# Performance work log

Hardware: AMD Instinct MI355X
Metric: run time of the kernel (lower is better)

Reference implementation:

```python
import jax, jax.numpy as jnp
import numpy as np
import math

NUM_LAYERS = 2
D_MODEL = 512
NUM_HEADS = 8
DFF = 2048
TIME_DIM = 8
B = 8
L = 512


def _ffn2(t, w1, b1, w2, b2):
    # gsm_ffn: two Dense(time_dim) layers, both with relu
    h = jax.nn.relu(t @ w1 + b1)
    return jax.nn.relu(h @ w2 + b2)


def _layer_norm(x, g, b, eps=1e-6):
    m = jnp.mean(x, axis=-1, keepdims=True)
    v = jnp.mean(jnp.square(x - m), axis=-1, keepdims=True)
    return (x - m) / jnp.sqrt(v + eps) * g + b


def _forward(x, t, wq, bq, wk, bk, wv, bv, wo, bo, w1, b1, w2, b2,
             ln1g, ln1b, ln2g, ln2b, pw1, pb1, pw2, pb2,
             sw1, sb1, sw2, sb2, bw1, bb1, bw2, bb2):
    Bn, Ln, D = x.shape
    H = NUM_HEADS
    dh = D // H
    scale = jnp.sqrt(jnp.float32(dh))
    two_pi = jnp.float32(2.0 * math.pi)
    for i in range(NUM_LAYERS):
        # ---- TimeGSMKernel: Gibbs spectral-mixture time kernel [B,L,L] ----
        pv = _ffn2(t, pw1[i], pb1[i], pw2[i], pb2[i])            # [B,L,td]
        tp = two_pi * pv * t                                      # [B,L,td]
        cos_enc = jnp.cos(tp[:, :, None, :] - tp[:, None, :, :])  # [B,L,L,td]
        sg = _ffn2(t, sw1[i], sb1[i], sw2[i], sb2[i]) + 1e-6      # [B,L,td]
        sq = sg[:, :, None, :]                                    # [B,L,1,td]
        sk = sg[:, None, :, :]                                    # [B,1,L,td]
        denom = sq * sq + sk * sk
        diff = t[:, :, None, :] - t[:, None, :, :]                # [B,L,L,1]
        exp_enc = jnp.exp(-(diff * diff) / denom)                 # [B,L,L,td]
        local_enc = jnp.sqrt(2.0 * sq * sk / denom)
        be = _ffn2(t, bw1[i], bb1[i], bw2[i], bb2[i])             # [B,L,td]
        kern = jnp.sum(be[:, :, None, :] * be[:, None, :, :]
                       * local_enc * exp_enc * cos_enc, axis=-1)  # [B,L,L]

        # ---- multi-head self-attention with kernel bias ----
        def heads(z):
            return z.reshape(Bn, Ln, H, dh).transpose(0, 2, 1, 3)
        q = heads(x @ wq[i] + bq[i])
        k = heads(x @ wk[i] + bk[i])
        v = heads(x @ wv[i] + bv[i])
        logits = jnp.einsum('bhqd,bhkd->bhqk', q, k) / scale
        logits = logits + (kern / jnp.exp(scale))[:, None, :, :]
        aw = jax.nn.softmax(logits, axis=-1)
        ctx = jnp.einsum('bhqk,bhkd->bhqd', aw, v)
        ctx = ctx.transpose(0, 2, 1, 3).reshape(Bn, Ln, D)
        attn_out = ctx @ wo[i] + bo[i]
        x = _layer_norm(x + attn_out, ln1g[i], ln1b[i])
        # ---- pointwise FFN (relu then linear) ----
        f = jax.nn.relu(x @ w1[i] + b1[i]) @ w2[i] + b2[i]
        x = _layer_norm(x + f, ln2g[i], ln2b[i])
    return x


def setup_inputs() -> dict:
    key = jax.random.key(0)
    ks = iter(jax.random.split(key, 40))
    def nrm(shape, s=0.02):
        return (jax.random.normal(next(ks), shape) * s).astype(jnp.float32)
    NL, D, TD = NUM_LAYERS, D_MODEL, TIME_DIM
    d = {
        'x': jax.random.normal(next(ks), (B, L, D), dtype=jnp.float32),
        't': jax.random.uniform(next(ks), (B, L, 1), dtype=jnp.float32),
        'wq': nrm((NL, D, D)), 'bq': jnp.zeros((NL, D), jnp.float32),
        'wk': nrm((NL, D, D)), 'bk': jnp.zeros((NL, D), jnp.float32),
        'wv': nrm((NL, D, D)), 'bv': jnp.zeros((NL, D), jnp.float32),
        'wo': nrm((NL, D, D)), 'bo': jnp.zeros((NL, D), jnp.float32),
        'w1': nrm((NL, D, DFF)), 'b1': jnp.zeros((NL, DFF), jnp.float32),
        'w2': nrm((NL, DFF, D)), 'b2': jnp.zeros((NL, D), jnp.float32),
        'ln1g': jnp.ones((NL, D), jnp.float32), 'ln1b': jnp.zeros((NL, D), jnp.float32),
        'ln2g': jnp.ones((NL, D), jnp.float32), 'ln2b': jnp.zeros((NL, D), jnp.float32),
        'pw1': nrm((NL, 1, TD), 0.5), 'pb1': 0.1 * jnp.ones((NL, TD), jnp.float32),
        'pw2': nrm((NL, TD, TD), 0.3), 'pb2': 0.1 * jnp.ones((NL, TD), jnp.float32),
        'sw1': nrm((NL, 1, TD), 0.5), 'sb1': 0.1 * jnp.ones((NL, TD), jnp.float32),
        'sw2': nrm((NL, TD, TD), 0.3), 'sb2': 0.5 * jnp.ones((NL, TD), jnp.float32),
        'bw1': nrm((NL, 1, TD), 0.5), 'bb1': 0.1 * jnp.ones((NL, TD), jnp.float32),
        'bw2': nrm((NL, TD, TD), 0.3), 'bb2': 0.1 * jnp.ones((NL, TD), jnp.float32),
    }
    return d


def reference(x, t, wq, bq, wk, bk, wv, bv, wo, bo, w1, b1, w2, b2,
              ln1g, ln1b, ln2g, ln2b, pw1, pb1, pw2, pb2,
              sw1, sb1, sw2, sb2, bw1, bb1, bw2, bb2):
    return _forward(x, t, wq, bq, wk, bk, wv, bv, wo, bo, w1, b1, w2, b2,
                    ln1g, ln1b, ln2g, ln2b, pw1, pb1, pw2, pb2,
                    sw1, sb1, sw2, sb2, bw1, bb1, bw2, bb2)
```

## Files before the change

kernel.cpp:

```cpp
#include <hip/hip_runtime.h>
#include <hip/hip_bf16.h>

#define DEV_INLINE __device__ __forceinline__

constexpr int NLAYERS = 2;
constexpr int DM = 512;
constexpr int NH = 8;
constexpr int DHD = 64;
constexpr int FF = 2048;
constexpr int TD = 8;
constexpr int BB = 8;
constexpr int LL = 512;
constexpr int ROWS = BB * LL;
constexpr int QKVN = 3 * DM;

constexpr float TWO_PI_F = 6.28318530717958647692f;
constexpr float INV_E8 = 3.3546262790251185e-4f;

typedef __attribute__((ext_vector_type(8))) short short8v;
typedef __attribute__((ext_vector_type(4))) float f32x4;

DEV_INLINE unsigned short bf16_rne(float x) {
  unsigned int u = __float_as_uint(x);
  unsigned int r = (u + 0x7fffu + ((u >> 16) & 1u)) >> 16;
  return (unsigned short)r;
}
DEV_INLINE float bf16_to_f(unsigned short h) {
  return __uint_as_float(((unsigned int)h) << 16);
}
DEV_INLINE void split_bf16(float x, unsigned short& h, unsigned short& l) {
  h = bf16_rne(x);
  float lo = x - bf16_to_f(h);
  l = bf16_rne(lo);
}

DEV_INLINE void ffn2_small(float tv,
                           const float* __restrict__ w1, const float* __restrict__ b1,
                           const float* __restrict__ w2, const float* __restrict__ b2,
                           float* out) {
  float h[TD];
#pragma unroll
  for (int d = 0; d < TD; ++d) h[d] = fmaxf(tv * w1[d] + b1[d], 0.f);
#pragma unroll
  for (int j = 0; j < TD; ++j) {
    float acc = b2[j];
#pragma unroll
    for (int d = 0; d < TD; ++d) acc += h[d] * w2[d * TD + j];
    out[j] = fmaxf(acc, 0.f);
  }
}

__global__ __launch_bounds__(256) void small_ffn_kernel(
    const float* __restrict__ t,
    const float* __restrict__ pw1, const float* __restrict__ pb1,
    const float* __restrict__ pw2, const float* __restrict__ pb2,
    const float* __restrict__ sw1, const float* __restrict__ sb1,
    const float* __restrict__ sw2, const float* __restrict__ sb2,
    const float* __restrict__ bw1, const float* __restrict__ bb1,
    const float* __restrict__ bw2, const float* __restrict__ bb2,
    float* __restrict__ tp, float* __restrict__ sg, float* __restrict__ be) {
  const int i = blockIdx.x * 256 + threadIdx.x;
  if (i >= ROWS) return;
  const float tv = t[i];
  float o[TD];
  ffn2_small(tv, pw1, pb1, pw2, pb2, o);
#pragma unroll
  for (int d = 0; d < TD; ++d) tp[(size_t)i * TD + d] = TWO_PI_F * o[d] * tv;
  ffn2_small(tv, sw1, sb1, sw2, sb2, o);
#pragma unroll
  for (int d = 0; d < TD; ++d) sg[(size_t)i * TD + d] = o[d] + 1e-6f;
  ffn2_small(tv, bw1, bb1, bw2, bb2, o);
#pragma unroll
  for (int d = 0; d < TD; ++d) be[(size_t)i * TD + d] = o[d];
}

DEV_INLINE void load8(const float* __restrict__ p, float* o) {
  float4 a = *reinterpret_cast<const float4*>(p);
  float4 b = *reinterpret_cast<const float4*>(p + 4);
  o[0] = a.x; o[1] = a.y; o[2] = a.z; o[3] = a.w;
  o[4] = b.x; o[5] = b.y; o[6] = b.z; o[7] = b.w;
}

__global__ __launch_bounds__(256) void kern_kernel(
    const float* __restrict__ t, const float* __restrict__ tp,
    const float* __restrict__ sg, const float* __restrict__ be,
    float* __restrict__ kernS) {
  const int k = blockIdx.x * 256 + threadIdx.x;
  const int q = blockIdx.y;
  const int b = blockIdx.z;
  const size_t iq = (size_t)b * LL + q;
  const size_t ik = (size_t)b * LL + k;
  const float tq = t[iq], tk = t[ik];
  const float diff = tq - tk;
  const float d2 = diff * diff;

  float tpq[TD], sgq[TD], beq[TD], tpk[TD], sgk[TD], bek[TD];
  load8(tp + iq * TD, tpq);
  load8(sg + iq * TD, sgq);
  load8(be + iq * TD, beq);
  load8(tp + ik * TD, tpk);
  load8(sg + ik * TD, sgk);
  load8(be + ik * TD, bek);

  float acc = 0.f;
#pragma unroll
  for (int d = 0; d < TD; ++d) {
    const float sq = sgq[d], sk = sgk[d];
    const float denom = sq * sq + sk * sk;
    const float inv = 1.0f / denom;
    const float e = __expf(-d2 * inv);
    const float loc = sqrtf(2.0f * sq * sk * inv);
    const float c = __cosf(tpq[d] - tpk[d]);
    acc += beq[d] * bek[d] * loc * e * c;
  }
  kernS[((size_t)b * LL + q) * LL + k] = acc * INV_E8;
}

__global__ __launch_bounds__(256) void td_kernel(
    const float* __restrict__ W, unsigned short* __restrict__ Thi,
    unsigned short* __restrict__ Tlo, int K, int N) {
  __shared__ float tile[32][33];
  const int k0 = blockIdx.x * 32, n0 = blockIdx.y * 32;
  const int tx = threadIdx.x & 31, ty = threadIdx.x >> 5;
#pragma unroll
  for (int i = 0; i < 4; ++i)
    tile[ty + i * 8][tx] = W[(size_t)(k0 + ty + i * 8) * N + n0 + tx];
  __syncthreads();
#pragma unroll
  for (int i = 0; i < 4; ++i) {
    const int n = n0 + ty + i * 8;
    const float v = tile[tx][ty + i * 8];
    unsigned short h, l;
    split_bf16(v, h, l);
    Thi[(size_t)n * K + k0 + tx] = h;
    Tlo[(size_t)n * K + k0 + tx] = l;
  }
}

__global__ __launch_bounds__(256) void decomp_kernel(
    const float* __restrict__ X, unsigned short* __restrict__ Hi,
    unsigned short* __restrict__ Lo, int n4) {
  const int i = blockIdx.x * 256 + threadIdx.x;
  if (i >= n4) return;
  const float4 v = *reinterpret_cast<const float4*>(X + (size_t)i * 4);
  unsigned short h0, h1, h2, h3, l0, l1, l2, l3;
  split_bf16(v.x, h0, l0);
  split_bf16(v.y, h1, l1);
  split_bf16(v.z, h2, l2);
  split_bf16(v.w, h3, l3);
  uint2 hv, lv;
  hv.x = (unsigned)h0 | ((unsigned)h1 << 16);
  hv.y = (unsigned)h2 | ((unsigned)h3 << 16);
  lv.x = (unsigned)l0 | ((unsigned)l1 << 16);
  lv.y = (unsigned)l2 | ((unsigned)l3 << 16);
  *reinterpret_cast<uint2*>(Hi + (size_t)i * 4) = hv;
  *reinterpret_cast<uint2*>(Lo + (size_t)i * 4) = lv;
}

__global__ __launch_bounds__(256) void qkvbias_kernel(
    const float* __restrict__ bq, const float* __restrict__ bk,
    const float* __restrict__ bv, float* __restrict__ out) {
  const int i = blockIdx.x * 256 + threadIdx.x;
  if (i >= QKVN) return;
  out[i] = i < DM ? bq[i] : (i < 2 * DM ? bk[i - DM] : bv[i - 2 * DM]);
}

template <int BN, bool RELU, bool SPLIT_OUT>
__global__ __launch_bounds__(256) void gemm_mfma(
    const unsigned short* __restrict__ Ahi, const unsigned short* __restrict__ Alo,
    const unsigned short* __restrict__ Bhi, const unsigned short* __restrict__ Blo,
    const float* __restrict__ bias, float* __restrict__ C,
    unsigned short* __restrict__ Chi, unsigned short* __restrict__ Clo,
    int M, int N, int K) {
  constexpr int BM = 128, BK = 32;
  constexpr int WT_M = 64;
  constexpr int WT_N = BN / 2;
  constexpr int MI = WT_M / 16;
  constexpr int NI = WT_N / 16;
  constexpr int A_IT = BM * BK / (256 * 8);
  constexpr int B_IT = BN * BK / (256 * 8);

  __shared__ unsigned short AsH[2][BM * BK];
  __shared__ unsigned short AsL[2][BM * BK];
  __shared__ unsigned short BsH[2][BN * BK];
  __shared__ unsigned short BsL[2][BN * BK];

  const int nwg = gridDim.x * gridDim.y;
  const int orig = blockIdx.y * gridDim.x + blockIdx.x;
  const int swz = (orig & 7) * (nwg >> 3) + (orig >> 3);
  const int bx = swz % gridDim.x;
  const int by = swz / gridDim.x;

  const int tid = threadIdx.x;
  const int lane = tid & 63;
  const int wid = tid >> 6;
  const int wr = wid >> 1, wc = wid & 1;
  const int rowBase = by * BM;
  const int colBase = bx * BN;
  const int l15 = lane & 15, l4 = lane >> 4;

  const int sg_ = tid & 3;
  const int srA = tid >> 2;
  const int swg = sg_ ^ (srA & 3) ^ ((srA >> 2) & 3);

  f32x4 acc[MI][NI] = {};
  const int nt = K / BK;

  uint4 ahR[A_IT], alR[A_IT], bhR[B_IT], blR[B_IT];

  auto loadRegs = [&](int kt) {
    const int k0 = kt * BK;
#pragma unroll
    for (int it = 0; it < A_IT; ++it) {
      const size_t base = (size_t)(rowBase + it * 64 + srA) * K + k0 + sg_ * 8;
      ahR[it] = *reinterpret_cast<const uint4*>(Ahi + base);
      alR[it] = *reinterpret_cast<const uint4*>(Alo + base);
    }
#pragma unroll
    for (int it = 0; it < B_IT; ++it) {
      const size_t base = (size_t)(colBase + it * 64 + srA) * K + k0 + sg_ * 8;
      bhR[it] = *reinterpret_cast<const uint4*>(Bhi + base);
      blR[it] = *reinterpret_cast<const uint4*>(Blo + base);
    }
  };

  auto writeLDS = [&](int buf) {
#pragma unroll
    for (int it = 0; it < A_IT; ++it) {
      const int off = ((it * 64 + srA) << 5) + (swg << 3);
      *reinterpret_cast<uint4*>(&AsH[buf][off]) = ahR[it];
      *reinterpret_cast<uint4*>(&AsL[buf][off]) = alR[it];
    }
#pragma unroll
    for (int it = 0; it < B_IT; ++it) {
      const int off = ((it * 64 + srA) << 5) + (swg << 3);
      *reinterpret_cast<uint4*>(&BsH[buf][off]) = bhR[it];
      *reinterpret_cast<uint4*>(&BsL[buf][off]) = blR[it];
    }
  };

  loadRegs(0);
  writeLDS(0);
  if (nt > 1) loadRegs(1);

  for (int t = 0; t < nt; ++t) {
    __syncthreads();
    const int cur = t & 1;
    if (t + 1 < nt) writeLDS(cur ^ 1);
    if (t + 2 < nt) loadRegs(t + 2);

    short8v ah[MI], al[MI], bh[NI], bl[NI];
#pragma unroll
    for (int mi = 0; mi < MI; ++mi) {
      const int r = wr * WT_M + mi * 16 + l15;
      const int g = l4 ^ (r & 3) ^ ((r >> 2) & 3);
      const int off = (r << 5) + (g << 3);
      ah[mi] = *reinterpret_cast<const short8v*>(&AsH[cur][off]);
      al[mi] = *reinterpret_cast<const short8v*>(&AsL[cur][off]);
    }
#pragma unroll
    for (int ni = 0; ni < NI; ++ni) {
      const int r = wc * WT_N + ni * 16 + l15;
      const int g = l4 ^ (r & 3) ^ ((r >> 2) & 3);
      const int off = (r << 5) + (g << 3);
      bh[ni] = *reinterpret_cast<const short8v*>(&BsH[cur][off]);
      bl[ni] = *reinterpret_cast<const short8v*>(&BsL[cur][off]);
    }
#pragma unroll
    for (int mi = 0; mi < MI; ++mi)
#pragma unroll
      for (int ni = 0; ni < NI; ++ni) {
        acc[mi][ni] = __builtin_amdgcn_mfma_f32_16x16x32_bf16(ah[mi], bh[ni], acc[mi][ni], 0, 0, 0);
        acc[mi][ni] = __builtin_amdgcn_mfma_f32_16x16x32_bf16(al[mi], bh[ni], acc[mi][ni], 0, 0, 0);
        acc[mi][ni] = __builtin_amdgcn_mfma_f32_16x16x32_bf16(ah[mi], bl[ni], acc[mi][ni], 0, 0, 0);
      }
  }

#pragma unroll
  for (int mi = 0; mi < MI; ++mi) {
#pragma unroll
    for (int ni = 0; ni < NI; ++ni) {
      const int col = colBase + wc * WT_N + ni * 16 + l15;
      const float bv = bias[col];
#pragma unroll
      for (int j = 0; j < 4; ++j) {
        const int row = rowBase + wr * WT_M + mi * 16 + l4 * 4 + j;
        float v = acc[mi][ni][j] + bv;
        if (RELU) v = fmaxf(v, 0.f);
        if (SPLIT_OUT) {
          unsigned short h, l;
          split_bf16(v, h, l);
          Chi[(size_t)row * N + col] = h;
          Clo[(size_t)row * N + col] = l;
        } else {
          C[(size_t)row * N + col] = v;
        }
      }
    }
  }
}

__global__ __launch_bounds__(256) void txp_kernel(
    const float* __restrict__ qkvb, float* __restrict__ ktb) {
  __shared__ float tile[32][33];
  const int bh = blockIdx.z;
  const int b = bh >> 3, h = bh & 7;
  const int kk0 = blockIdx.x * 32, d0 = blockIdx.y * 32;
  const int tx = threadIdx.x & 31, ty = threadIdx.x >> 5;
#pragma unroll
  for (int i = 0; i < 4; ++i) {
    const int kk = kk0 + ty + i * 8;
    tile[ty + i * 8][tx] = qkvb[(size_t)(b * LL + kk) * QKVN + DM + h * DHD + d0 + tx];
  }
  __syncthreads();
#pragma unroll
  for (int i = 0; i < 4; ++i) {
    const int d = d0 + ty + i * 8;
    ktb[((size_t)bh * DHD + d) * LL + kk0 + tx] = tile[tx][ty + i * 8];
  }
}

constexpr int TQ = 8;

__global__ __launch_bounds__(256) void attn_kernel(
    const float* __restrict__ qkvb, const float* __restrict__ ktb,
    const float* __restrict__ kernS,
    unsigned short* __restrict__ ctxhi, unsigned short* __restrict__ ctxlo) {
  const int id = blockIdx.x + 8 * (blockIdx.y + 64 * blockIdx.z);
  const int w = (id & 7) * 512 + (id >> 3);
  const int h = w & 7;
  const int qt = (w >> 3) & 63;
  const int b = w >> 9;
  const int tid = threadIdx.x;
  const int q0 = qt * TQ;

  __shared__ float qst[DHD][TQ];
  __shared__ float lst[LL][12];
  __shared__ float red[4][TQ][DHD];
  __shared__ float invS[TQ];

  {
    const int d = tid & 63;
    const int qq0 = tid >> 6;
#pragma unroll
    for (int rep = 0; rep < 2; ++rep) {
      const int qq = qq0 + rep * 4;
      qst[d][qq] = qkvb[(size_t)(b * LL + q0 + qq) * QKVN + h * DHD + d];
    }
  }
  __syncthreads();

  {
    const int kk = tid;
    const float* kcol = ktb + (size_t)(b * NH + h) * DHD * LL;
    float dot0[TQ] = {}, dot1[TQ] = {};
#pragma unroll 4
    for (int d = 0; d < DHD; ++d) {
      const float ka = kcol[(size_t)d * LL + kk];
      const float kb2 = kcol[(size_t)d * LL + kk + 256];
      const float4 qa = *reinterpret_cast<const float4*>(&qst[d][0]);
      const float4 qb2 = *reinterpret_cast<const float4*>(&qst[d][4]);
      dot0[0] += qa.x * ka; dot0[1] += qa.y * ka; dot0[2] += qa.z * ka; dot0[3] += qa.w * ka;
      dot0[4] += qb2.x * ka; dot0[5] += qb2.y * ka; dot0[6] += qb2.z * ka; dot0[7] += qb2.w * ka;
      dot1[0] += qa.x * kb2; dot1[1] += qa.y * kb2; dot1[2] += qa.z * kb2; dot1[3] += qa.w * kb2;
      dot1[4] += qb2.x * kb2; dot1[5] += qb2.y * kb2; dot1[6] += qb2.z * kb2; dot1[7] += qb2.w * kb2;
    }
#pragma unroll
    for (int qq = 0; qq < TQ; ++qq) {
      const size_t kbase = ((size_t)b * LL + q0 + qq) * LL;
      dot0[qq] = dot0[qq] * 0.125f + kernS[kbase + kk];
      dot1[qq] = dot1[qq] * 0.125f + kernS[kbase + kk + 256];
    }
    float4 p;
    p.x = dot0[0]; p.y = dot0[1]; p.z = dot0[2]; p.w = dot0[3];
    *reinterpret_cast<float4*>(&lst[kk][0]) = p;
    p.x = dot0[4]; p.y = dot0[5]; p.z = dot0[6]; p.w = dot0[7];
    *reinterpret_cast<float4*>(&lst[kk][4]) = p;
    p.x = dot1[0]; p.y = dot1[1]; p.z = dot1[2]; p.w = dot1[3];
    *reinterpret_cast<float4*>(&lst[kk + 256][0]) = p;
    p.x = dot1[4]; p.y = dot1[5]; p.z = dot1[6]; p.w = dot1[7];
    *reinterpret_cast<float4*>(&lst[kk + 256][4]) = p;
  }
  __syncthreads();

  {
    const int row = tid >> 5;
    const int l32 = tid & 31;
    float m = -1e30f;
#pragma unroll
    for (int j = 0; j < 16; ++j) m = fmaxf(m, lst[l32 + j * 32][row]);
#pragma unroll
    for (int s = 16; s; s >>= 1) m = fmaxf(m, __shfl_xor(m, s, 32));
    float sum = 0.f;
#pragma unroll
    for (int j = 0; j < 16; ++j) {
      const float e = __expf(lst[l32 + j * 32][row] - m);
      lst[l32 + j * 32][row] = e;
      sum += e;
    }
#pragma unroll
    for (int s = 16; s; s >>= 1) sum += __shfl_xor(sum, s, 32);
    if (l32 == 0) invS[row] = 1.0f / sum;
  }
  __syncthreads();

  const int d = tid & 63;
  const int c = tid >> 6;
  float acc[TQ] = {};
  {
    const float* vbase = qkvb + (size_t)(b * LL) * QKVN + 2 * DM + h * DHD + d;
    for (int kk = c * 128; kk < c * 128 + 128; ++kk) {
      const float vv = vbase[(size_t)kk * QKVN];
      const float4 pa = *reinterpret_cast<const float4*>(&lst[kk][0]);
      const float4 pb2 = *reinterpret_cast<const float4*>(&lst[kk][4]);
      acc[0] += pa.x * vv; acc[1] += pa.y * vv; acc[2] += pa.z * vv; acc[3] += pa.w * vv;
      acc[4] += pb2.x * vv; acc[5] += pb2.y * vv; acc[6] += pb2.z * vv; acc[7] += pb2.w * vv;
    }
  }
#pragma unroll
  for (int qq = 0; qq < TQ; ++qq) red[c][qq][d] = acc[qq];
  __syncthreads();
  if (c == 0) {
#pragma unroll
    for (int qq = 0; qq < TQ; ++qq) {
      const float r = ((red[0][qq][d] + red[1][qq][d]) + (red[2][qq][d] + red[3][qq][d])) * invS[qq];
      unsigned short hh, ll;
      split_bf16(r, hh, ll);
      const size_t o = (size_t)(b * LL + q0 + qq) * DM + h * DHD + d;
      ctxhi[o] = hh;
      ctxlo[o] = ll;
    }
  }
}

__global__ __launch_bounds__(256) void resid_ln_kernel(
    const float* __restrict__ X, const float* __restrict__ R,
    const float* __restrict__ g, const float* __restrict__ bta,
    float* __restrict__ Out, unsigned short* __restrict__ OutHi,
    unsigned short* __restrict__ OutLo) {
  const int row = blockIdx.x * 4 + (threadIdx.x >> 6);
  const int lane = threadIdx.x & 63;
  const float* x = X + (size_t)row * DM;
  const float* r = R + (size_t)row * DM;

  float v[8];
  float s = 0.f;
#pragma unroll
  for (int j = 0; j < 2; ++j) {
    const float4 a = *reinterpret_cast<const float4*>(x + lane * 8 + j * 4);
    const float4 c = *reinterpret_cast<const float4*>(r + lane * 8 + j * 4);
    v[j * 4 + 0] = a.x + c.x;
    v[j * 4 + 1] = a.y + c.y;
    v[j * 4 + 2] = a.z + c.z;
    v[j * 4 + 3] = a.w + c.w;
    s += v[j * 4 + 0] + v[j * 4 + 1] + v[j * 4 + 2] + v[j * 4 + 3];
  }
#pragma unroll
  for (int m = 1; m < 64; m <<= 1) s += __shfl_xor(s, m, 64);
  const float mean = s * (1.f / DM);
  float var = 0.f;
#pragma unroll
  for (int j = 0; j < 8; ++j) {
    const float dlt = v[j] - mean;
    var += dlt * dlt;
  }
#pragma unroll
  for (int m = 1; m < 64; m <<= 1) var += __shfl_xor(var, m, 64);
  var *= (1.f / DM);
  const float inv = 1.0f / sqrtf(var + 1e-6f);

  unsigned short hs[8], ls[8];
#pragma unroll
  for (int j = 0; j < 2; ++j) {
    const float4 gg = *reinterpret_cast<const float4*>(g + lane * 8 + j * 4);
    const float4 bb = *reinterpret_cast<const float4*>(bta + lane * 8 + j * 4);
    float4 o;
    o.x = (v[j * 4 + 0] - mean) * inv * gg.x + bb.x;
    o.y = (v[j * 4 + 1] - mean) * inv * gg.y + bb.y;
    o.z = (v[j * 4 + 2] - mean) * inv * gg.z + bb.z;
    o.w = (v[j * 4 + 3] - mean) * inv * gg.w + bb.w;
    *reinterpret_cast<float4*>(Out + (size_t)row * DM + lane * 8 + j * 4) = o;
    split_bf16(o.x, hs[j * 4 + 0], ls[j * 4 + 0]);
    split_bf16(o.y, hs[j * 4 + 1], ls[j * 4 + 1]);
    split_bf16(o.z, hs[j * 4 + 2], ls[j * 4 + 2]);
    split_bf16(o.w, hs[j * 4 + 3], ls[j * 4 + 3]);
  }
  uint4 hv, lv;
  hv.x = (unsigned)hs[0] | ((unsigned)hs[1] << 16);
  hv.y = (unsigned)hs[2] | ((unsigned)hs[3] << 16);
  hv.z = (unsigned)hs[4] | ((unsigned)hs[5] << 16);
  hv.w = (unsigned)hs[6] | ((unsigned)hs[7] << 16);
  lv.x = (unsigned)ls[0] | ((unsigned)ls[1] << 16);
  lv.y = (unsigned)ls[2] | ((unsigned)ls[3] << 16);
  lv.z = (unsigned)ls[4] | ((unsigned)ls[5] << 16);
  lv.w = (unsigned)ls[6] | ((unsigned)ls[7] << 16);
  *reinterpret_cast<uint4*>(OutHi + (size_t)row * DM + lane * 8) = hv;
  *reinterpret_cast<uint4*>(OutLo + (size_t)row * DM + lane * 8) = lv;
}

extern "C" void kernel_launch(void* const* d_in, const int* in_sizes, int n_in,
                              void* d_out, int out_size, void* d_ws, size_t ws_size,
                              hipStream_t stream) {
  const float* x_in = (const float*)d_in[0];
  const float* t = (const float*)d_in[1];
  const float* wq = (const float*)d_in[2];
  const float* bq = (const float*)d_in[3];
  const float* wk = (const float*)d_in[4];
  const float* bk = (const float*)d_in[5];
  const float* wv = (const float*)d_in[6];
  const float* bv = (const float*)d_in[7];
  const float* wo = (const float*)d_in[8];
  const float* bo = (const float*)d_in[9];
  const float* w1 = (const float*)d_in[10];
  const float* b1 = (const float*)d_in[11];
  const float* w2 = (const float*)d_in[12];
  const float* b2 = (const float*)d_in[13];
  const float* ln1g = (const float*)d_in[14];
  const float* ln1b = (const float*)d_in[15];
  const float* ln2g = (const float*)d_in[16];
  const float* ln2b = (const float*)d_in[17];
  const float* pw1 = (const float*)d_in[18];
  const float* pb1 = (const float*)d_in[19];
  const float* pw2 = (const float*)d_in[20];
  const float* pb2 = (const float*)d_in[21];
  const float* sw1 = (const float*)d_in[22];
  const float* sb1 = (const float*)d_in[23];
  const float* sw2 = (const float*)d_in[24];
  const float* sb2 = (const float*)d_in[25];
  const float* bw1 = (const float*)d_in[26];
  const float* bb1 = (const float*)d_in[27];
  const float* bw2 = (const float*)d_in[28];
  const float* bb2 = (const float*)d_in[29];

  char* wsb = (char*)d_ws;
  size_t off = 0;
  auto allocB = [&](size_t bytes) {
    char* p = wsb + off;
    off += (bytes + 255) & ~(size_t)255;
    return p;
  };
  float* tpb = (float*)allocB(ROWS * TD * 4);
  float* sgb = (float*)allocB(ROWS * TD * 4);
  float* beb = (float*)allocB(ROWS * TD * 4);
  float* kernS = (float*)allocB((size_t)BB * LL * LL * 4);
  float* qkvb = (float*)allocB((size_t)ROWS * QKVN * 4);
  float* ktb = (float*)allocB((size_t)BB * NH * DHD * LL * 4);
  float* ao = (float*)allocB((size_t)ROWS * DM * 4);
  float* xb = (float*)allocB((size_t)ROWS * DM * 4);
  float* fb = (float*)allocB((size_t)ROWS * DM * 4);
  float* xn = (float*)allocB((size_t)ROWS * DM * 4);
  float* qkvbias = (float*)allocB(QKVN * 4);
  unsigned short* qkvwt_hi = (unsigned short*)allocB((size_t)QKVN * DM * 2);
  unsigned short* qkvwt_lo = (unsigned short*)allocB((size_t)QKVN * DM * 2);
  unsigned short* wot_hi = (unsigned short*)allocB((size_t)DM * DM * 2);
  unsigned short* wot_lo = (unsigned short*)allocB((size_t)DM * DM * 2);
  unsigned short* w1t_hi = (unsigned short*)allocB((size_t)FF * DM * 2);
  unsigned short* w1t_lo = (unsigned short*)allocB((size_t)FF * DM * 2);
  unsigned short* w2t_hi = (unsigned short*)allocB((size_t)DM * FF * 2);
  unsigned short* w2t_lo = (unsigned short*)allocB((size_t)DM * FF * 2);
  unsigned short* xhi = (unsigned short*)allocB((size_t)ROWS * DM * 2);
  unsigned short* xlo = (unsigned short*)allocB((size_t)ROWS * DM * 2);
  unsigned short* ctxhi = (unsigned short*)allocB((size_t)ROWS * DM * 2);
  unsigned short* ctxlo = (unsigned short*)allocB((size_t)ROWS * DM * 2);
  unsigned short* hhi = (unsigned short*)qkvb;
  unsigned short* hlo = hhi + (size_t)ROWS * FF;

  const float* xcur = x_in;

  for (int i = 0; i < NLAYERS; ++i) {
    td_kernel<<<dim3(16, 16), 256, 0, stream>>>(wq + (size_t)i * DM * DM, qkvwt_hi, qkvwt_lo, DM, DM);
    td_kernel<<<dim3(16, 16), 256, 0, stream>>>(wk + (size_t)i * DM * DM, qkvwt_hi + (size_t)DM * DM, qkvwt_lo + (size_t)DM * DM, DM, DM);
    td_kernel<<<dim3(16, 16), 256, 0, stream>>>(wv + (size_t)i * DM * DM, qkvwt_hi + (size_t)2 * DM * DM, qkvwt_lo + (size_t)2 * DM * DM, DM, DM);
    td_kernel<<<dim3(16, 16), 256, 0, stream>>>(wo + (size_t)i * DM * DM, wot_hi, wot_lo, DM, DM);
    td_kernel<<<dim3(16, 64), 256, 0, stream>>>(w1 + (size_t)i * DM * FF, w1t_hi, w1t_lo, DM, FF);
    td_kernel<<<dim3(64, 16), 256, 0, stream>>>(w2 + (size_t)i * FF * DM, w2t_hi, w2t_lo, FF, DM);
    qkvbias_kernel<<<(QKVN + 255) / 256, 256, 0, stream>>>(bq + i * DM, bk + i * DM, bv + i * DM, qkvbias);

    small_ffn_kernel<<<ROWS / 256, 256, 0, stream>>>(
        t, pw1 + i * TD, pb1 + i * TD, pw2 + i * TD * TD, pb2 + i * TD,
        sw1 + i * TD, sb1 + i * TD, sw2 + i * TD * TD, sb2 + i * TD,
        bw1 + i * TD, bb1 + i * TD, bw2 + i * TD * TD, bb2 + i * TD,
        tpb, sgb, beb);
    kern_kernel<<<dim3(LL / 256, LL, BB), 256, 0, stream>>>(t, tpb, sgb, beb, kernS);

    if (i == 0) {
      decomp_kernel<<<(ROWS * DM / 4 + 255) / 256, 256, 0, stream>>>(x_in, xhi, xlo, ROWS * DM / 4);
    }

    gemm_mfma<128, false, false><<<dim3(QKVN / 128, ROWS / 128), 256, 0, stream>>>(
        xhi, xlo, qkvwt_hi, qkvwt_lo, qkvbias, qkvb, nullptr, nullptr, ROWS, QKVN, DM);

    txp_kernel<<<dim3(LL / 32, DHD / 32, BB * NH), 256, 0, stream>>>(qkvb, ktb);

    attn_kernel<<<dim3(NH, LL / TQ, BB), 256, 0, stream>>>(qkvb, ktb, kernS, ctxhi, ctxlo);

    gemm_mfma<64, false, false><<<dim3(DM / 64, ROWS / 128), 256, 0, stream>>>(
        ctxhi, ctxlo, wot_hi, wot_lo, bo + i * DM, ao, nullptr, nullptr, ROWS, DM, DM);

    resid_ln_kernel<<<ROWS / 4, 256, 0, stream>>>(
        xcur, ao, ln1g + i * DM, ln1b + i * DM, xb, xhi, xlo);

    gemm_mfma<128, true, true><<<dim3(FF / 128, ROWS / 128), 256, 0, stream>>>(
        xhi, xlo, w1t_hi, w1t_lo, b1 + i * FF, nullptr, hhi, hlo, ROWS, FF, DM);

    gemm_mfma<64, false, false><<<dim3(DM / 64, ROWS / 128), 256, 0, stream>>>(
        hhi, hlo, w2t_hi, w2t_lo, b2 + i * DM, fb, nullptr, nullptr, ROWS, DM, FF);

    float* ln2_out = (i == NLAYERS - 1) ? (float*)d_out : xn;
    resid_ln_kernel<<<ROWS / 4, 256, 0, stream>>>(
        xb, fb, ln2g + i * DM, ln2b + i * DM, ln2_out, xhi, xlo);

    xcur = xn;
  }
}
```

Baseline: 872.5 us.

## Move attention QK and PV products onto bf16x3 MFMA with split QKV output

The QKV GEMM now writes split bf16 hi/lo output instead of fp32. The scalar fp32 attention kernel is replaced by an MFMA kernel that does QK^T and P·V with three-term bf16 split products. The K transpose is dropped and a V transpose into hi/lo buffers is added, and each block now covers 16 queries instead of 8. This targets the scalar FMA cost of attention, which was a large part of runtime, in exchange for precision that depends on the hi/lo split and more shared-memory traffic for the softmax probabilities.

```diff
diff --git a/kernel.cpp b/kernel.cpp
--- a/kernel.cpp
+++ b/kernel.cpp
@@ -300,9 +300,10 @@
   }
 }
 
-__global__ __launch_bounds__(256) void txp_kernel(
-    const float* __restrict__ qkvb, float* __restrict__ ktb) {
-  __shared__ float tile[32][33];
+__global__ __launch_bounds__(256) void vtxp_kernel(
+    const unsigned short* __restrict__ qkvhi, const unsigned short* __restrict__ qkvlo,
+    unsigned short* __restrict__ vtbhi, unsigned short* __restrict__ vtblo) {
+  __shared__ unsigned short th[32][33], tl[32][33];
   const int bh = blockIdx.z;
   const int b = bh >> 3, h = bh & 7;
   const int kk0 = blockIdx.x * 32, d0 = blockIdx.y * 32;
@@ -310,125 +311,120 @@
 #pragma unroll
   for (int i = 0; i < 4; ++i) {
     const int kk = kk0 + ty + i * 8;
-    tile[ty + i * 8][tx] = qkvb[(size_t)(b * LL + kk) * QKVN + DM + h * DHD + d0 + tx];
+    const size_t src = (size_t)(b * LL + kk) * QKVN + 2 * DM + h * DHD + d0 + tx;
+    th[ty + i * 8][tx] = qkvhi[src];
+    tl[ty + i * 8][tx] = qkvlo[src];
   }
   __syncthreads();
 #pragma unroll
   for (int i = 0; i < 4; ++i) {
     const int d = d0 + ty + i * 8;
-    ktb[((size_t)bh * DHD + d) * LL + kk0 + tx] = tile[tx][ty + i * 8];
-  }
-}
-
-constexpr int TQ = 8;
-
-__global__ __launch_bounds__(256) void attn_kernel(
-    const float* __restrict__ qkvb, const float* __restrict__ ktb,
+    const size_t dst = ((size_t)bh * DHD + d) * LL + kk0 + tx;
+    vtbhi[dst] = th[tx][ty + i * 8];
+    vtblo[dst] = tl[tx][ty + i * 8];
+  }
+}
+
+constexpr int ATQ = 16;
+
+__global__ __launch_bounds__(256) void attn_mfma(
+    const unsigned short* __restrict__ qkvhi, const unsigned short* __restrict__ qkvlo,
+    const unsigned short* __restrict__ vtbhi, const unsigned short* __restrict__ vtblo,
     const float* __restrict__ kernS,
     unsigned short* __restrict__ ctxhi, unsigned short* __restrict__ ctxlo) {
-  const int id = blockIdx.x + 8 * (blockIdx.y + 64 * blockIdx.z);
-  const int w = (id & 7) * 512 + (id >> 3);
+  const int id = blockIdx.x;
+  const int w = (id & 7) * 256 + (id >> 3);
   const int h = w & 7;
-  const int qt = (w >> 3) & 63;
-  const int b = w >> 9;
+  const int qt = (w >> 3) & 31;
+  const int b = w >> 8;
   const int tid = threadIdx.x;
-  const int q0 = qt * TQ;
-
-  __shared__ float qst[DHD][TQ];
-  __shared__ float lst[LL][12];
-  __shared__ float red[4][TQ][DHD];
-  __shared__ float invS[TQ];
-
+  const int lane = tid & 63;
+  const int wv = tid >> 6;
+  const int l15 = lane & 15, l4 = lane >> 4;
+  const int q0 = qt * ATQ;
+
+  __shared__ float S[ATQ][521];
+  __shared__ unsigned short Phi[ATQ][520];
+  __shared__ unsigned short Plo[ATQ][520];
+  __shared__ float sinv[ATQ];
+
+  short8v qh[2], ql[2];
   {
-    const int d = tid & 63;
-    const int qq0 = tid >> 6;
-#pragma unroll
-    for (int rep = 0; rep < 2; ++rep) {
-      const int qq = qq0 + rep * 4;
-      qst[d][qq] = qkvb[(size_t)(b * LL + q0 + qq) * QKVN + h * DHD + d];
+    const size_t qbase = (size_t)(b * LL + q0 + l15) * QKVN + h * DHD;
+#pragma unroll
+    for (int ks = 0; ks < 2; ++ks) {
+      qh[ks] = *reinterpret_cast<const short8v*>(qkvhi + qbase + ks * 32 + l4 * 8);
+      ql[ks] = *reinterpret_cast<const short8v*>(qkvlo + qbase + ks * 32 + l4 * 8);
+    }
+  }
+
+  for (int nt = 0; nt < 8; ++nt) {
+    const int kk0 = wv * 128 + nt * 16;
+    const size_t kbase = (size_t)(b * LL + kk0 + l15) * QKVN + DM + h * DHD;
+    f32x4 acc = {};
+#pragma unroll
+    for (int ks = 0; ks < 2; ++ks) {
+      const short8v kh = *reinterpret_cast<const short8v*>(qkvhi + kbase + ks * 32 + l4 * 8);
+      const short8v kl = *reinterpret_cast<const short8v*>(qkvlo + kbase + ks * 32 + l4 * 8);
+      acc = __builtin_amdgcn_mfma_f32_16x16x32_bf16(qh[ks], kh, acc, 0, 0, 0);
+      acc = __builtin_amdgcn_mfma_f32_16x16x32_bf16(ql[ks], kh, acc, 0, 0, 0);
+      acc = __builtin_amdgcn_mfma_f32_16x16x32_bf16(qh[ks], kl, acc, 0, 0, 0);
+    }
+#pragma unroll
+    for (int j = 0; j < 4; ++j) {
+      const int row = l4 * 4 + j;
+      S[row][kk0 + l15] =
+          acc[j] * 0.125f + kernS[((size_t)b * LL + q0 + row) * LL + kk0 + l15];
     }
   }
   __syncthreads();
 
   {
-    const int kk = tid;
-    const float* kcol = ktb + (size_t)(b * NH + h) * DHD * LL;
-    float dot0[TQ] = {}, dot1[TQ] = {};
-#pragma unroll 4
-    for (int d = 0; d < DHD; ++d) {
-      const float ka = kcol[(size_t)d * LL + kk];
-      const float kb2 = kcol[(size_t)d * LL + kk + 256];
-      const float4 qa = *reinterpret_cast<const float4*>(&qst[d][0]);
-      const float4 qb2 = *reinterpret_cast<const float4*>(&qst[d][4]);
-      dot0[0] += qa.x * ka; dot0[1] += qa.y * ka; dot0[2] += qa.z * ka; dot0[3] += qa.w * ka;
-      dot0[4] += qb2.x * ka; dot0[5] += qb2.y * ka; dot0[6] += qb2.z * ka; dot0[7] += qb2.w * ka;
-      dot1[0] += qa.x * kb2; dot1[1] += qa.y * kb2; dot1[2] += qa.z * kb2; dot1[3] += qa.w * kb2;
-      dot1[4] += qb2.x * kb2; dot1[5] += qb2.y * kb2; dot1[6] += qb2.z * kb2; dot1[7] += qb2.w * kb2;
-    }
-#pragma unroll
-    for (int qq = 0; qq < TQ; ++qq) {
-      const size_t kbase = ((size_t)b * LL + q0 + qq) * LL;
-      dot0[qq] = dot0[qq] * 0.125f + kernS[kbase + kk];
-      dot1[qq] = dot1[qq] * 0.125f + kernS[kbase + kk + 256];
-    }
-    float4 p;
-    p.x = dot0[0]; p.y = dot0[1]; p.z = dot0[2]; p.w = dot0[3];
-    *reinterpret_cast<float4*>(&lst[kk][0]) = p;
-    p.x = dot0[4]; p.y = dot0[5]; p.z = dot0[6]; p.w = dot0[7];
-    *reinterpret_cast<float4*>(&lst[kk][4]) = p;
-    p.x = dot1[0]; p.y = dot1[1]; p.z = dot1[2]; p.w = dot1[3];
-    *reinterpret_cast<float4*>(&lst[kk + 256][0]) = p;
-    p.x = dot1[4]; p.y = dot1[5]; p.z = dot1[6]; p.w = dot1[7];
-    *reinterpret_cast<float4*>(&lst[kk + 256][4]) = p;
+    const int r = tid >> 4, c = tid & 15;
+    float m = -1e30f;
+#pragma unroll
+    for (int j = 0; j < 32; ++j) m = fmaxf(m, S[r][c + j * 16]);
+#pragma unroll
+    for (int s = 8; s; s >>= 1) m = fmaxf(m, __shfl_xor(m, s, 16));
+    float sum = 0.f;
+#pragma unroll
+    for (int j = 0; j < 32; ++j) {
+      const float e = __expf(S[r][c + j * 16] - m);
+      unsigned short hh, ll;
+      split_bf16(e, hh, ll);
+      Phi[r][c + j * 16] = hh;
+      Plo[r][c + j * 16] = ll;
+      sum += e;
+    }
+#pragma unroll
+    for (int s = 8; s; s >>= 1) sum += __shfl_xor(sum, s, 16);
+    if (c == 0) sinv[r] = 1.0f / sum;
   }
   __syncthreads();
 
   {
-    const int row = tid >> 5;
-    const int l32 = tid & 31;
-    float m = -1e30f;
-#pragma unroll
-    for (int j = 0; j < 16; ++j) m = fmaxf(m, lst[l32 + j * 32][row]);
-#pragma unroll
-    for (int s = 16; s; s >>= 1) m = fmaxf(m, __shfl_xor(m, s, 32));
-    float sum = 0.f;
-#pragma unroll
-    for (int j = 0; j < 16; ++j) {
-      const float e = __expf(lst[l32 + j * 32][row] - m);
-      lst[l32 + j * 32][row] = e;
-      sum += e;
-    }
-#pragma unroll
-    for (int s = 16; s; s >>= 1) sum += __shfl_xor(sum, s, 32);
-    if (l32 == 0) invS[row] = 1.0f / sum;
-  }
-  __syncthreads();
-
-  const int d = tid & 63;
-  const int c = tid >> 6;
-  float acc[TQ] = {};
-  {
-    const float* vbase = qkvb + (size_t)(b * LL) * QKVN + 2 * DM + h * DHD + d;
-    for (int kk = c * 128; kk < c * 128 + 128; ++kk) {
-      const float vv = vbase[(size_t)kk * QKVN];
-      const float4 pa = *reinterpret_cast<const float4*>(&lst[kk][0]);
-      const float4 pb2 = *reinterpret_cast<const float4*>(&lst[kk][4]);
-      acc[0] += pa.x * vv; acc[1] += pa.y * vv; acc[2] += pa.z * vv; acc[3] += pa.w * vv;
-      acc[4] += pb2.x * vv; acc[5] += pb2.y * vv; acc[6] += pb2.z * vv; acc[7] += pb2.w * vv;
-    }
-  }
-#pragma unroll
-  for (int qq = 0; qq < TQ; ++qq) red[c][qq][d] = acc[qq];
-  __syncthreads();
-  if (c == 0) {
-#pragma unroll
-    for (int qq = 0; qq < TQ; ++qq) {
-      const float r = ((red[0][qq][d] + red[1][qq][d]) + (red[2][qq][d] + red[3][qq][d])) * invS[qq];
+    const int d0 = wv * 16;
+    const size_t vbase = ((size_t)(b * NH + h) * DHD + d0 + l15) * LL;
+    f32x4 acc = {};
+    for (int kt = 0; kt < 16; ++kt) {
+      const int kk0 = kt * 32;
+      const short8v ph = *reinterpret_cast<const short8v*>(&Phi[l15][kk0 + l4 * 8]);
+      const short8v pl = *reinterpret_cast<const short8v*>(&Plo[l15][kk0 + l4 * 8]);
+      const short8v vh = *reinterpret_cast<const short8v*>(vtbhi + vbase + kk0 + l4 * 8);
+      const short8v vl = *reinterpret_cast<const short8v*>(vtblo + vbase + kk0 + l4 * 8);
+      acc = __builtin_amdgcn_mfma_f32_16x16x32_bf16(ph, vh, acc, 0, 0, 0);
+      acc = __builtin_amdgcn_mfma_f32_16x16x32_bf16(pl, vh, acc, 0, 0, 0);
+      acc = __builtin_amdgcn_mfma_f32_16x16x32_bf16(ph, vl, acc, 0, 0, 0);
+    }
+#pragma unroll
+    for (int j = 0; j < 4; ++j) {
+      const int row = l4 * 4 + j;
+      const float o = acc[j] * sinv[row];
       unsigned short hh, ll;
-      split_bf16(r, hh, ll);
-      const size_t o = (size_t)(b * LL + q0 + qq) * DM + h * DHD + d;
-      ctxhi[o] = hh;
-      ctxlo[o] = ll;
+      split_bf16(o, hh, ll);
+      const size_t oo = (size_t)(b * LL + q0 + row) * DM + h * DHD + d0 + l15;
+      ctxhi[oo] = hh;
+      ctxlo[oo] = ll;
     }
   }
 }
@@ -543,8 +539,11 @@
   float* sgb = (float*)allocB(ROWS * TD * 4);
   float* beb = (float*)allocB(ROWS * TD * 4);
   float* kernS = (float*)allocB((size_t)BB * LL * LL * 4);
-  float* qkvb = (float*)allocB((size_t)ROWS * QKVN * 4);
-  float* ktb = (float*)allocB((size_t)BB * NH * DHD * LL * 4);
+  unsigned short* qkvhi = (unsigned short*)allocB(
+      ((size_t)ROWS * QKVN * 2 + (size_t)BB * NH * DHD * LL * 2) * 2);
+  unsigned short* qkvlo = qkvhi + (size_t)ROWS * QKVN;
+  unsigned short* vtbhi = qkvlo + (size_t)ROWS * QKVN;
+  unsigned short* vtblo = vtbhi + (size_t)BB * NH * DHD * LL;
   float* ao = (float*)allocB((size_t)ROWS * DM * 4);
   float* xb = (float*)allocB((size_t)ROWS * DM * 4);
   float* fb = (float*)allocB((size_t)ROWS * DM * 4);
@@ -562,7 +561,7 @@
   unsigned short* xlo = (unsigned short*)allocB((size_t)ROWS * DM * 2);
   unsigned short* ctxhi = (unsigned short*)allocB((size_t)ROWS * DM * 2);
   unsigned short* ctxlo = (unsigned short*)allocB((size_t)ROWS * DM * 2);
-  unsigned short* hhi = (unsigned short*)qkvb;
+  unsigned short* hhi = qkvhi;
   unsigned short* hlo = hhi + (size_t)ROWS * FF;
 
   const float* xcur = x_in;
@@ -587,12 +586,14 @@
       decomp_kernel<<<(ROWS * DM / 4 + 255) / 256, 256, 0, stream>>>(x_in, xhi, xlo, ROWS * DM / 4);
     }
 
-    gemm_mfma<128, false, false><<<dim3(QKVN / 128, ROWS / 128), 256, 0, stream>>>(
-        xhi, xlo, qkvwt_hi, qkvwt_lo, qkvbias, qkvb, nullptr, nullptr, ROWS, QKVN, DM);
-
-    txp_kernel<<<dim3(LL / 32, DHD / 32, BB * NH), 256, 0, stream>>>(qkvb, ktb);
-
-    attn_kernel<<<dim3(NH, LL / TQ, BB), 256, 0, stream>>>(qkvb, ktb, kernS, ctxhi, ctxlo);
+    gemm_mfma<128, false, true><<<dim3(QKVN / 128, ROWS / 128), 256, 0, stream>>>(
+        xhi, xlo, qkvwt_hi, qkvwt_lo, qkvbias, nullptr, qkvhi, qkvlo, ROWS, QKVN, DM);
+
+    vtxp_kernel<<<dim3(LL / 32, DHD / 32, BB * NH), 256, 0, stream>>>(
+        qkvhi, qkvlo, vtbhi, vtblo);
+
+    attn_mfma<<<dim3(BB * NH * (LL / ATQ)), 256, 0, stream>>>(
+        qkvhi, qkvlo, vtbhi, vtblo, kernS, ctxhi, ctxlo);
 
     gemm_mfma<64, false, false><<<dim3(DM / 64, ROWS / 128), 256, 0, stream>>>(
         ctxhi, ctxlo, wot_hi, wot_lo, bo + i * DM, ao, nullptr, nullptr, ROWS, DM, DM);
```

Result: faster. 851.2 us (-2.4%).
